# Optimization experiments

Measured on AMD Instinct MI355X. Metric: run time of the kernel, lower is better.

Reference implementation:

```python
import jax, jax.numpy as jnp
import numpy as np

D_MODEL = 768
NHEAD = 12
HEAD_DIM = D_MODEL // NHEAD


def setup_inputs() -> dict:
    key = jax.random.key(0)
    ks = jax.random.split(key, 5)
    B, S = 1, 4096
    x = jax.random.normal(ks[0], (B, S, D_MODEL), dtype=jnp.float32)
    # Linear params (stored as [in, out] so y = x @ W + b)
    s_in = 1.0 / np.sqrt(D_MODEL)
    W_qkv = jax.random.uniform(ks[1], (D_MODEL, 3 * D_MODEL), minval=-s_in, maxval=s_in, dtype=jnp.float32)
    b_qkv = jax.random.uniform(ks[2], (3 * D_MODEL,), minval=-s_in, maxval=s_in, dtype=jnp.float32)
    W_o = jax.random.uniform(ks[3], (D_MODEL, D_MODEL), minval=-s_in, maxval=s_in, dtype=jnp.float32)
    b_o = jax.random.uniform(ks[4], (D_MODEL,), minval=-s_in, maxval=s_in, dtype=jnp.float32)
    return {"x": x, "W_qkv": W_qkv, "b_qkv": b_qkv, "W_o": W_o, "b_o": b_o}


def reference(x, W_qkv, b_qkv, W_o, b_o):
    B, S, _ = x.shape
    qkv = x @ W_qkv + b_qkv                      # [B,S,3D]
    qkv = qkv.reshape(B, S, 3, NHEAD, HEAD_DIM)
    q, k, v = qkv[:, :, 0], qkv[:, :, 1], qkv[:, :, 2]   # [B,S,H,hd]
    scale = D_MODEL ** (-0.5)                    # NOTE: d_model, not head_dim
    scores = jnp.einsum('bqhd,bkhd->bhqk', q, k) * scale
    attn = jax.nn.softmax(scores, axis=-1)
    out = jnp.einsum('bhqk,bkhd->bqhd', attn, v) * HEAD_DIM  # custom post-softmax rescale
    out = out.reshape(B, S, D_MODEL)
    return out @ W_o + b_o
```

## Files before the change

### kernel.cpp

```cpp
#include <hip/hip_runtime.h>
#include <stdint.h>
#include <math.h>

typedef unsigned short u16;
typedef __attribute__((ext_vector_type(8))) __bf16 bf16x8;
typedef __attribute__((ext_vector_type(4))) float f32x4;
typedef __attribute__((ext_vector_type(16))) float f32x16;
typedef __attribute__((ext_vector_type(4))) short short4v;
typedef __attribute__((ext_vector_type(4))) float float4v;
typedef __attribute__((ext_vector_type(2))) uint32_t u32x2;
typedef __attribute__((ext_vector_type(4))) uint32_t u32x4;

#define SEQ 4096
#define DM 768
#define NH 12

__device__ __forceinline__ u16 f2b(float f) {
  uint32_t u = __float_as_uint(f);
  uint32_t r = (u + 0x7fffu + ((u >> 16) & 1u)) >> 16;
  return (u16)r;
}

__device__ __forceinline__ uint32_t cvtpk(float lo, float hi) {
  uint32_t r;
  asm("v_cvt_pk_bf16_f32 %0, %1, %2" : "=v"(r) : "v"(lo), "v"(hi));
  return r;
}

__device__ __forceinline__ void gload16(const void* g, void* l) {
  __builtin_amdgcn_global_load_lds(
      (const __attribute__((address_space(1))) void*)g,
      (__attribute__((address_space(3))) void*)l, 16, 0, 0);
}

__device__ __forceinline__ f32x4 mfma16(bf16x8 a, bf16x8 b, f32x4 c) {
  return __builtin_amdgcn_mfma_f32_16x16x32_bf16(a, b, c, 0, 0, 0);
}

__device__ __forceinline__ f32x16 mfma32(bf16x8 a, bf16x8 b, f32x16 c) {
  return __builtin_amdgcn_mfma_f32_32x32x16_bf16(a, b, c, 0, 0, 0);
}

__device__ __forceinline__ float pexp2(float x) {
  return fmaf(fmaf(fmaf(0.0571709f, x, 0.249989f), x, 0.6927303f), x, 0.9987737f);
}

__global__ __launch_bounds__(256) void k_conv(const float* __restrict__ in,
                                              u16* __restrict__ out) {
  int i = blockIdx.x * 256 + threadIdx.x;
  float4v v = ((const float4v*)in)[i];
  short4v o;
  o.x = (short)f2b(v.x);
  o.y = (short)f2b(v.y);
  o.z = (short)f2b(v.z);
  o.w = (short)f2b(v.w);
  ((short4v*)out)[i] = o;
}

__global__ __launch_bounds__(256) void k_transconv(const float* __restrict__ in,
                                                   u16* __restrict__ out,
                                                   int R, int C) {
  __shared__ float tile[32][33];
  int tx = threadIdx.x & 31, ty = threadIdx.x >> 5;
  int r0 = blockIdx.y * 32, c0 = blockIdx.x * 32;
#pragma unroll
  for (int k = 0; k < 4; ++k)
    tile[ty + 8 * k][tx] = in[(size_t)(r0 + ty + 8 * k) * C + c0 + tx];
  __syncthreads();
#pragma unroll
  for (int k = 0; k < 4; ++k)
    out[(size_t)(c0 + ty + 8 * k) * R + r0 + tx] = f2b(tile[tx][ty + 8 * k]);
}

template <int EPI>
__global__ __launch_bounds__(256) void k_gemm(
    const u16* __restrict__ A, const u16* __restrict__ Bt,
    const float* __restrict__ bias, float* __restrict__ Cf,
    u16* __restrict__ qh, u16* __restrict__ kh, u16* __restrict__ vT,
    int M, int N, int K) {
  __shared__ u16 sA[128 * 64];
  __shared__ u16 sB[128 * 64];
  const int tid = threadIdx.x;
  const int w = tid >> 6, l = tid & 63;
  const int wr = w >> 1, wc = w & 1;
  const int lg = l >> 4, lc = l & 15;
  const int row0 = blockIdx.y * 128, col0 = blockIdx.x * 128;
  const int trg = tid >> 3;
  const int cg = ((tid & 7) ^ (trg & 7)) * 8;
  char* ldsA = (char*)sA + (w << 10);
  char* ldsB = (char*)sB + (w << 10);
  f32x4 acc[4][4] = {};
  for (int ks = 0; ks < K; ks += 64) {
#pragma unroll
    for (int i = 0; i < 4; ++i) {
      gload16(A + (size_t)(row0 + i * 32 + trg) * K + ks + cg, ldsA + i * 4096);
      gload16(Bt + (size_t)(col0 + i * 32 + trg) * K + ks + cg, ldsB + i * 4096);
    }
    __syncthreads();
#pragma unroll
    for (int kk = 0; kk < 2; ++kk) {
      bf16x8 af[4], bfr[4];
#pragma unroll
      for (int m = 0; m < 4; ++m)
        af[m] = *(const bf16x8*)&sA[(wr * 64 + m * 16 + lc) * 64 +
                                    (((kk << 2) + lg) ^ (lc & 7)) * 8];
#pragma unroll
      for (int n = 0; n < 4; ++n)
        bfr[n] = *(const bf16x8*)&sB[(wc * 64 + n * 16 + lc) * 64 +
                                     (((kk << 2) + lg) ^ (lc & 7)) * 8];
#pragma unroll
      for (int m = 0; m < 4; ++m)
#pragma unroll
        for (int n = 0; n < 4; ++n)
          acc[m][n] = mfma16(af[m], bfr[n], acc[m][n]);
    }
    __syncthreads();
  }
  const float QSC = 0.036084391824351615f * 1.4426950408889634f;
#pragma unroll
  for (int m = 0; m < 4; ++m) {
    const int grow0 = row0 + wr * 64 + m * 16 + lg * 4;
#pragma unroll
    for (int n = 0; n < 4; ++n) {
      const int gcol = col0 + wc * 64 + n * 16 + lc;
      const float bb = bias[gcol];
      if (EPI == 1) {
#pragma unroll
        for (int r = 0; r < 4; ++r)
          Cf[(size_t)(grow0 + r) * N + gcol] = acc[m][n][r] + bb;
      } else {
        const int typ = gcol / DM;
        const int hd = gcol % DM;
        const int h = hd >> 6, d = hd & 63;
        if (typ == 2) {
          u32x2 pk2;
          pk2.x = cvtpk(acc[m][n][0] + bb, acc[m][n][1] + bb);
          pk2.y = cvtpk(acc[m][n][2] + bb, acc[m][n][3] + bb);
          *(u32x2*)&vT[(size_t)(h * 64 + d) * SEQ + grow0] = pk2;
        } else if (typ == 0) {
#pragma unroll
          for (int r = 0; r < 4; ++r)
            qh[((size_t)h * SEQ + grow0 + r) * 64 + d] = f2b((acc[m][n][r] + bb) * QSC);
        } else {
          const int lgp = ((lg & 1) << 1) | (lg >> 1);
          const int growp = row0 + wr * 64 + m * 16 + lgp * 4;
#pragma unroll
          for (int r = 0; r < 4; ++r)
            kh[((size_t)h * SEQ + growp + r) * 64 + d] = f2b(acc[m][n][r] + bb);
        }
      }
    }
  }
}

__global__ __launch_bounds__(256, 3) void k_attn(
    const u16* __restrict__ qh, const u16* __restrict__ kh,
    const u16* __restrict__ vT, u16* __restrict__ att) {
  __shared__ alignas(16) u16 smem[5 * 4096];
  u16* const sQ = smem;
  u16* const sK0 = smem + 4096;
  u16* const sK1 = smem + 2 * 4096;
  u16* const sV0 = smem + 3 * 4096;
  u16* const sV1 = smem + 4 * 4096;
  const int tid = threadIdx.x;
  const int w = tid >> 6, l = tid & 63;
  const int l31 = l & 31, hi = l >> 5;
  const int khalf = w & 1, qhf = w >> 1;
  const int h = blockIdx.y;
  const int q0 = blockIdx.x * 64;
  const int tr8 = tid >> 3;
  const int cc = ((tid & 7) ^ (tr8 & 7)) * 8;
  const u16* Qg = qh + ((size_t)h * SEQ + q0) * 64;
  const u16* Kg = kh + (size_t)h * SEQ * 64;
  const u16* Vg = vT + (size_t)h * 64 * SEQ;
  gload16(Qg + (size_t)tr8 * 64 + cc, (char*)sQ + (w << 10));
  gload16(Qg + (size_t)(32 + tr8) * 64 + cc, (char*)sQ + 4096 + (w << 10));
  gload16(Kg + (size_t)tr8 * 64 + cc, (char*)sK0 + (w << 10));
  gload16(Kg + (size_t)(32 + tr8) * 64 + cc, (char*)sK0 + 4096 + (w << 10));
  gload16(Vg + (size_t)tr8 * SEQ + cc, (char*)sV0 + (w << 10));
  gload16(Vg + (size_t)(32 + tr8) * SEQ + cc, (char*)sV0 + 4096 + (w << 10));
  __syncthreads();
  const int qrow = qhf * 32 + l31;
  const int krow = khalf * 32 + l31;
  bf16x8 qf[4];
#pragma unroll
  for (int ds = 0; ds < 4; ++ds)
    qf[ds] = *(const bf16x8*)&sQ[qrow * 64 + (((ds << 1) + hi) ^ (qrow & 7)) * 8];
  f32x16 oacc0 = {}, oacc1 = {};
  float l_r = 0.f;

  auto body = [&](const u16* sKc, const u16* sVc, char* nK, char* nV, int t) {
    if (t < 63) {
      const int k1 = (t + 1) * 64;
      gload16(Kg + (size_t)(k1 + tr8) * 64 + cc, nK + (w << 10));
      gload16(Kg + (size_t)(k1 + 32 + tr8) * 64 + cc, nK + 4096 + (w << 10));
      gload16(Vg + (size_t)tr8 * SEQ + k1 + cc, nV + (w << 10));
      gload16(Vg + (size_t)(32 + tr8) * SEQ + k1 + cc, nV + 4096 + (w << 10));
    }
    f32x16 sa = {};
    __builtin_amdgcn_s_setprio(1);
#pragma unroll
    for (int ds = 0; ds < 4; ++ds) {
      bf16x8 kf = *(const bf16x8*)&sKc[krow * 64 + (((ds << 1) + hi) ^ (krow & 7)) * 8];
      sa = mfma32(kf, qf[ds], sa);
    }
    __builtin_amdgcn_s_setprio(0);
    float p[16];
#pragma unroll
    for (int r = 0; r < 16; ++r) p[r] = pexp2(sa[r]);
    l_r += (((p[0] + p[1]) + (p[2] + p[3])) + ((p[4] + p[5]) + (p[6] + p[7]))) +
           (((p[8] + p[9]) + (p[10] + p[11])) + ((p[12] + p[13]) + (p[14] + p[15])));
    u32x4 w0v, w1v;
    w0v.x = cvtpk(p[0], p[1]);
    w0v.y = cvtpk(p[2], p[3]);
    w0v.z = cvtpk(p[4], p[5]);
    w0v.w = cvtpk(p[6], p[7]);
    w1v.x = cvtpk(p[8], p[9]);
    w1v.y = cvtpk(p[10], p[11]);
    w1v.z = cvtpk(p[12], p[13]);
    w1v.w = cvtpk(p[14], p[15]);
    const bf16x8 pf0 = __builtin_bit_cast(bf16x8, w0v);
    const bf16x8 pf1 = __builtin_bit_cast(bf16x8, w1v);
    __builtin_amdgcn_s_setprio(1);
    {
      const int vr0 = l31, vr1 = 32 + l31;
      bf16x8 v00 = *(const bf16x8*)&sVc[vr0 * 64 + (((khalf << 2) + 0 + hi) ^ (vr0 & 7)) * 8];
      bf16x8 v01 = *(const bf16x8*)&sVc[vr0 * 64 + (((khalf << 2) + 2 + hi) ^ (vr0 & 7)) * 8];
      oacc0 = mfma32(v00, pf0, oacc0);
      oacc0 = mfma32(v01, pf1, oacc0);
      bf16x8 v10 = *(const bf16x8*)&sVc[vr1 * 64 + (((khalf << 2) + 0 + hi) ^ (vr1 & 7)) * 8];
      bf16x8 v11 = *(const bf16x8*)&sVc[vr1 * 64 + (((khalf << 2) + 2 + hi) ^ (vr1 & 7)) * 8];
      oacc1 = mfma32(v10, pf0, oacc1);
      oacc1 = mfma32(v11, pf1, oacc1);
    }
    __builtin_amdgcn_s_setprio(0);
    __syncthreads();
  };

  for (int t = 0; t < 64; t += 2) {
    body(sK0, sV0, (char*)sK1, (char*)sV1, t);
    body(sK1, sV1, (char*)sK0, (char*)sV0, t + 1);
  }

  l_r += __shfl_xor(l_r, 32);
  float* xch = (float*)smem;
  float* mySlot = xch + (w * 64 + l) * 17;
  const f32x16 owrite = khalf ? oacc0 : oacc1;
#pragma unroll
  for (int r = 0; r < 16; ++r) mySlot[r] = owrite[r];
  mySlot[16] = l_r;
  __syncthreads();
  const float* pSlot = xch + (((w ^ 1) * 64) + l) * 17;
  f32x16 okeep = khalf ? oacc1 : oacc0;
  const float lt = l_r + pSlot[16];
#pragma unroll
  for (int r = 0; r < 16; ++r) okeep[r] += pSlot[r];
  const float li = 64.0f / lt;
  u16* orow = att + (size_t)(q0 + qrow) * DM + h * 64 + khalf * 32 + hi * 4;
#pragma unroll
  for (int g = 0; g < 4; ++g) {
    u32x2 pk2;
    pk2.x = cvtpk(okeep[4 * g + 0] * li, okeep[4 * g + 1] * li);
    pk2.y = cvtpk(okeep[4 * g + 2] * li, okeep[4 * g + 3] * li);
    *(u32x2*)(orow + 8 * g) = pk2;
  }
}

extern "C" void kernel_launch(void* const* d_in, const int* in_sizes, int n_in,
                              void* d_out, int out_size, void* d_ws, size_t ws_size,
                              hipStream_t stream) {
  const float* x = (const float*)d_in[0];
  const float* W_qkv = (const float*)d_in[1];
  const float* b_qkv = (const float*)d_in[2];
  const float* W_o = (const float*)d_in[3];
  const float* b_o = (const float*)d_in[4];
  float* out = (float*)d_out;
  char* ws = (char*)d_ws;
  u16* x_bf = (u16*)(ws);
  u16* wqkvT = (u16*)(ws + 6291456);
  u16* woT = (u16*)(ws + 9830400);
  u16* qh = (u16*)(ws + 11010048);
  u16* kh = (u16*)(ws + 17301504);
  u16* vT = (u16*)(ws + 23592960);
  u16* att = (u16*)(ws + 29884416);

  k_conv<<<dim3(3072), dim3(256), 0, stream>>>(x, x_bf);
  k_transconv<<<dim3(72, 24), dim3(256), 0, stream>>>(W_qkv, wqkvT, DM, 3 * DM);
  k_transconv<<<dim3(24, 24), dim3(256), 0, stream>>>(W_o, woT, DM, DM);
  k_gemm<0><<<dim3(18, 32), dim3(256), 0, stream>>>(
      x_bf, wqkvT, b_qkv, nullptr, qh, kh, vT, SEQ, 3 * DM, DM);
  k_attn<<<dim3(64, 12), dim3(256), 0, stream>>>(qh, kh, vT, att);
  k_gemm<1><<<dim3(6, 32), dim3(256), 0, stream>>>(
      att, woT, b_o, out, nullptr, nullptr, nullptr, SEQ, DM, DM);
}
```

Baseline: 128.0 us.

## Add small-tile output GEMM and remap attention blocks across XCDs

Adds a 64x64-tile GEMM kernel for the output projection, launching 768 blocks instead of 192 so the 256 CUs get more blocks to work on. It also flattens the attention grid to 1D and permutes block IDs so that consecutive blocks, which round-robin across the 8 XCDs, land on the same head within an XCD. That should improve L2 reuse of K/V. The small tile has lower arithmetic intensity and no double buffering, so it loads more per FLOP.

```diff
diff --git a/kernel.cpp b/kernel.cpp
--- a/kernel.cpp
+++ b/kernel.cpp
@@ -153,6 +153,61 @@
   }
 }
 
+__global__ __launch_bounds__(256) void k_gemm_s(
+    const u16* __restrict__ A, const u16* __restrict__ Bt,
+    const float* __restrict__ bias, float* __restrict__ Cf,
+    int M, int N, int K) {
+  __shared__ u16 sA[64 * 64];
+  __shared__ u16 sB[64 * 64];
+  const int tid = threadIdx.x;
+  const int w = tid >> 6, l = tid & 63;
+  const int wr = w >> 1, wc = w & 1;
+  const int lg = l >> 4, lc = l & 15;
+  const int row0 = blockIdx.y * 64, col0 = blockIdx.x * 64;
+  const int trg = tid >> 3;
+  const int cg = ((tid & 7) ^ (trg & 7)) * 8;
+  char* ldsA = (char*)sA + (w << 10);
+  char* ldsB = (char*)sB + (w << 10);
+  f32x4 acc[2][2] = {};
+  for (int ks = 0; ks < K; ks += 64) {
+    gload16(A + (size_t)(row0 + trg) * K + ks + cg, ldsA);
+    gload16(A + (size_t)(row0 + 32 + trg) * K + ks + cg, ldsA + 4096);
+    gload16(Bt + (size_t)(col0 + trg) * K + ks + cg, ldsB);
+    gload16(Bt + (size_t)(col0 + 32 + trg) * K + ks + cg, ldsB + 4096);
+    __syncthreads();
+#pragma unroll
+    for (int kk = 0; kk < 2; ++kk) {
+      bf16x8 af[2], bfr[2];
+#pragma unroll
+      for (int m = 0; m < 2; ++m)
+        af[m] = *(const bf16x8*)&sA[(wr * 32 + m * 16 + lc) * 64 +
+                                    (((kk << 2) + lg) ^ (lc & 7)) * 8];
+#pragma unroll
+      for (int n = 0; n < 2; ++n)
+        bfr[n] = *(const bf16x8*)&sB[(wc * 32 + n * 16 + lc) * 64 +
+                                     (((kk << 2) + lg) ^ (lc & 7)) * 8];
+#pragma unroll
+      for (int m = 0; m < 2; ++m)
+#pragma unroll
+        for (int n = 0; n < 2; ++n)
+          acc[m][n] = mfma16(af[m], bfr[n], acc[m][n]);
+    }
+    __syncthreads();
+  }
+#pragma unroll
+  for (int m = 0; m < 2; ++m) {
+    const int grow0 = row0 + wr * 32 + m * 16 + lg * 4;
+#pragma unroll
+    for (int n = 0; n < 2; ++n) {
+      const int gcol = col0 + wc * 32 + n * 16 + lc;
+      const float bb = bias[gcol];
+#pragma unroll
+      for (int r = 0; r < 4; ++r)
+        Cf[(size_t)(grow0 + r) * N + gcol] = acc[m][n][r] + bb;
+    }
+  }
+}
+
 __global__ __launch_bounds__(256, 3) void k_attn(
     const u16* __restrict__ qh, const u16* __restrict__ kh,
     const u16* __restrict__ vT, u16* __restrict__ att) {
@@ -166,8 +221,10 @@
   const int w = tid >> 6, l = tid & 63;
   const int l31 = l & 31, hi = l >> 5;
   const int khalf = w & 1, qhf = w >> 1;
-  const int h = blockIdx.y;
-  const int q0 = blockIdx.x * 64;
+  const int fid = blockIdx.x;
+  const int swz = (fid & 7) * 96 + (fid >> 3);
+  const int h = swz >> 6;
+  const int q0 = (swz & 63) << 6;
   const int tr8 = tid >> 3;
   const int cc = ((tid & 7) ^ (tr8 & 7)) * 8;
   const u16* Qg = qh + ((size_t)h * SEQ + q0) * 64;
@@ -289,7 +346,7 @@
   k_transconv<<<dim3(24, 24), dim3(256), 0, stream>>>(W_o, woT, DM, DM);
   k_gemm<0><<<dim3(18, 32), dim3(256), 0, stream>>>(
       x_bf, wqkvT, b_qkv, nullptr, qh, kh, vT, SEQ, 3 * DM, DM);
-  k_attn<<<dim3(64, 12), dim3(256), 0, stream>>>(qh, kh, vT, att);
-  k_gemm<1><<<dim3(6, 32), dim3(256), 0, stream>>>(
-      att, woT, b_o, out, nullptr, nullptr, nullptr, SEQ, DM, DM);
-}
+  k_attn<<<dim3(768), dim3(256), 0, stream>>>(qh, kh, vT, att);
+  k_gemm_s<<<dim3(12, 64), dim3(256), 0, stream>>>(
+      att, woT, b_o, out, SEQ, DM, DM);
+}
```

Measured after the change: 119.8 us. 6.4% less time.
